# Optimization experiments

Measured on AMD Instinct MI355X. Metric: run time of the kernel, lower is better.

The kernel has to match this reference:

```python
import jax, jax.numpy as jnp
import numpy as np

N, D_IN, D_H = 8192, 512, 512


def setup_inputs() -> dict:
    key = jax.random.key(0)
    kH, kWq, kbq, kWk, kbk = jax.random.split(key, 5)
    s_in = 1.0 / np.sqrt(D_IN)
    return {
        "H": jax.random.normal(kH, (N, D_IN), dtype=jnp.float32),
        "Wq": jax.random.normal(kWq, (D_IN, D_H), dtype=jnp.float32) * s_in,
        "bq": jax.random.normal(kbq, (D_H,), dtype=jnp.float32) * 0.01,
        "Wk": jax.random.normal(kWk, (D_IN, D_H), dtype=jnp.float32) * s_in,
        "bk": jax.random.normal(kbk, (D_H,), dtype=jnp.float32) * 0.01,
    }


def reference(H, Wq, bq, Wk, bk):
    # H: [N, T]; Q, K: [N, d_h]
    Q = H @ Wq + bq
    K = H @ Wk + bk
    # A: [N, N] raw scores
    A = Q @ K.T
    n = A.shape[0]
    # torch.where(eye, 0, A): zero out the diagonal BEFORE scale/softmax
    A = A.at[jnp.arange(n), jnp.arange(n)].set(0.0)
    A = A / jnp.sqrt(jnp.asarray(K.shape[-1], A.dtype))
    A = jax.nn.softmax(A, axis=-1)
    # aggregate values (= H itself) and add residual
    return A @ H + H
```

## Files before the change

### kernel.cpp

```cpp
#include <hip/hip_runtime.h>
#include <cstdint>
#include <cstddef>

#define GLOBAL_AS __attribute__((address_space(1)))
#define LDS_AS __attribute__((address_space(3)))

typedef __attribute__((ext_vector_type(8))) short short8;
typedef __attribute__((ext_vector_type(4))) float floatx4;
typedef __attribute__((ext_vector_type(2))) long long2v;

#if defined(__has_builtin)
#if __has_builtin(__builtin_amdgcn_cvt_pk_fp8_f32)
#define HAVE_HW_FP8 1
#endif
#endif

static __device__ __forceinline__ unsigned short f2bf(float f) {
  uint32_t u = __builtin_bit_cast(uint32_t, f);
  u += 0x7fffu + ((u >> 16) & 1u);
  return (unsigned short)(u >> 16);
}

static __device__ __forceinline__ unsigned char f2fp8(float f) {
#ifdef HAVE_HW_FP8
  float c = fminf(fmaxf(f, -448.f), 448.f);
  return (unsigned char)(__builtin_amdgcn_cvt_pk_fp8_f32(c, 0.f, 0, false) & 0xff);
#else
  unsigned char s = 0;
  if (f < 0.f) { s = 0x80; f = -f; }
  if (f >= 448.f) return s | 0x7e;
  if (f < 0.015625f) { int r = (int)(f * 512.f + 0.5f); return s | (unsigned char)r; }
  uint32_t u = __builtin_bit_cast(uint32_t, f);
  int e = (int)((u >> 23) & 0xff) - 127;
  uint32_t keep = (u >> 20) & 7, rest = u & 0xfffffu;
  if (rest > 0x80000u || (rest == 0x80000u && (keep & 1))) ++keep;
  if (keep == 8) { keep = 0; ++e; }
  if (e > 8) return s | 0x7e;
  return s | (unsigned char)(((e + 7) << 3) | keep);
#endif
}

static __device__ __forceinline__ uint32_t pack4fp8(const float e[4]) {
#ifdef HAVE_HW_FP8
  const uint32_t p01 = (uint32_t)__builtin_amdgcn_cvt_pk_fp8_f32(e[0], e[1], 0, false);
  const uint32_t p23 = (uint32_t)__builtin_amdgcn_cvt_pk_fp8_f32(e[2], e[3], 0, false);
  return (p01 & 0xffffu) | (p23 << 16);
#else
  return (uint32_t)f2fp8(e[0]) | ((uint32_t)f2fp8(e[1]) << 8) |
         ((uint32_t)f2fp8(e[2]) << 16) | ((uint32_t)f2fp8(e[3]) << 24);
#endif
}

static __device__ __forceinline__ uint32_t gather_dword(uint32_t w, int quad, int l15) {
  const int src = quad * 16 + 4 * (l15 & 3);
  const int sh = (l15 >> 2) * 8;
  const uint32_t v0 = (uint32_t)__shfl((int)w, src);
  const uint32_t v1 = (uint32_t)__shfl((int)w, src + 1);
  const uint32_t v2 = (uint32_t)__shfl((int)w, src + 2);
  const uint32_t v3 = (uint32_t)__shfl((int)w, src + 3);
  return ((v0 >> sh) & 0xffu) | (((v1 >> sh) & 0xffu) << 8) |
         (((v2 >> sh) & 0xffu) << 16) | (((v3 >> sh) & 0xffu) << 24);
}

static __device__ __forceinline__ void wait_vm0() {
  __builtin_amdgcn_s_waitcnt(0x0f70);
}

__global__ __launch_bounds__(256) void transpose_h_kernel(
    const float* __restrict__ in, unsigned char* __restrict__ outT8,
    unsigned short* __restrict__ outN, int R, int C) {
  __shared__ float t[64][65];
  const int bc = blockIdx.x * 64;
  const int br = blockIdx.y * 64;
  const int tc = threadIdx.x & 63;
  const int tr = threadIdx.x >> 6;
  for (int r = tr; r < 64; r += 4) {
    const float v = in[(size_t)(br + r) * C + bc + tc];
    t[r][tc] = v;
    outN[(size_t)(br + r) * C + bc + tc] = f2bf(v);
  }
  __syncthreads();
  for (int r = tr; r < 64; r += 4)
    outT8[(size_t)(bc + r) * R + br + tc] = f2fp8(t[tc][r]);
}

__global__ __launch_bounds__(256) void transpose_w_kernel(
    const float* __restrict__ in, unsigned short* __restrict__ outT, int R, int C) {
  __shared__ float t[64][65];
  const int bc = blockIdx.x * 64;
  const int br = blockIdx.y * 64;
  const int tc = threadIdx.x & 63;
  const int tr = threadIdx.x >> 6;
  for (int r = tr; r < 64; r += 4)
    t[r][tc] = in[(size_t)(br + r) * C + bc + tc];
  __syncthreads();
  for (int r = tr; r < 64; r += 4)
    outT[(size_t)(bc + r) * R + br + tc] = f2bf(t[tc][r]);
}

__global__ __launch_bounds__(256) void pack_bias_kernel(
    const float* __restrict__ bq, const float* __restrict__ bk,
    float* __restrict__ bqk) {
  int i = blockIdx.x * 256 + threadIdx.x;
  bqk[i] = (i < 512) ? bq[i] : bk[i - 512];
}

__global__ __launch_bounds__(256, 4) void gemm_proj(
    const unsigned short* __restrict__ A,
    const unsigned short* __restrict__ Bt,
    int Ncols, int K,
    const float* __restrict__ bias,
    unsigned char* __restrict__ C8)
{
  __shared__ unsigned short As[2][128 * 32];
  __shared__ unsigned short Bs[2][128 * 32];

  const int tid  = threadIdx.x;
  const int lane = tid & 63;
  const int wave = tid >> 6;
  const int wr   = (wave >> 1) * 64;
  const int wc   = (wave & 1) * 64;
  const int quad = lane >> 4;
  const int l15  = lane & 15;
  const int bm   = blockIdx.y * 128;
  const int bn   = blockIdx.x * 128;

  const int c0 = tid, c1 = tid + 256;
  const int r0a = c0 >> 2, k0a = (c0 & 3) << 3;
  const int r1a = c1 >> 2, k1a = (c1 & 3) << 3;

  auto stage = [&](int kt, int b) {
    __builtin_amdgcn_global_load_lds(
        (const GLOBAL_AS void*)(A + (size_t)(bm + r0a) * K + kt + k0a),
        (LDS_AS void*)(&As[b][c0 * 8]), 16, 0, 0);
    __builtin_amdgcn_global_load_lds(
        (const GLOBAL_AS void*)(A + (size_t)(bm + r1a) * K + kt + k1a),
        (LDS_AS void*)(&As[b][c1 * 8]), 16, 0, 0);
    __builtin_amdgcn_global_load_lds(
        (const GLOBAL_AS void*)(Bt + (size_t)(bn + r0a) * K + kt + k0a),
        (LDS_AS void*)(&Bs[b][c0 * 8]), 16, 0, 0);
    __builtin_amdgcn_global_load_lds(
        (const GLOBAL_AS void*)(Bt + (size_t)(bn + r1a) * K + kt + k1a),
        (LDS_AS void*)(&Bs[b][c1 * 8]), 16, 0, 0);
  };

  floatx4 acc[4][4];
#pragma unroll
  for (int i = 0; i < 4; ++i)
#pragma unroll
    for (int j = 0; j < 4; ++j)
      acc[i][j] = (floatx4){0.f, 0.f, 0.f, 0.f};

  stage(0, 0);
  const int nIter = K >> 5;
  for (int it = 0; it < nIter; ++it) {
    const int b = it & 1;
    wait_vm0();
    __syncthreads();
    if (it + 1 < nIter) stage((it + 1) << 5, b ^ 1);

    short8 af[4], bfr[4];
#pragma unroll
    for (int i = 0; i < 4; ++i)
      af[i] = *(const short8*)(&As[b][(wr + i * 16 + l15) * 32 + quad * 8]);
#pragma unroll
    for (int j = 0; j < 4; ++j)
      bfr[j] = *(const short8*)(&Bs[b][(wc + j * 16 + l15) * 32 + quad * 8]);
#pragma unroll
    for (int i = 0; i < 4; ++i)
#pragma unroll
      for (int j = 0; j < 4; ++j)
        acc[i][j] = __builtin_amdgcn_mfma_f32_16x16x32_bf16(af[i], bfr[j], acc[i][j], 0, 0, 0);
  }

#pragma unroll
  for (int i = 0; i < 4; ++i) {
    const int rl = bm + wr + i * 16 + quad * 4;
#pragma unroll
    for (int r = 0; r < 4; ++r) {
      const int row = rl + r;
      float e[4];
#pragma unroll
      for (int j = 0; j < 4; ++j)
        e[j] = acc[i][j][r] + bias[bn + wc + j * 16 + l15];
      const uint32_t d = gather_dword(pack4fp8(e), quad, l15);
      *(uint32_t*)(C8 + (size_t)row * Ncols + bn + wc + 4 * l15) = d;
    }
  }
}

__global__ __launch_bounds__(512, 6) void gemm_qk8(
    const unsigned char* __restrict__ A,
    const unsigned char* __restrict__ Bt,
    int Ncols, int K, int lda, int ldb,
    float* __restrict__ lsum,
    int row0,
    unsigned char* __restrict__ P8)
{
  __shared__ unsigned char As[2][128 * 64];
  __shared__ unsigned char Bs[2][128 * 64];

  const int tid  = threadIdx.x;
  const int lane = tid & 63;
  const int wave = tid >> 6;
  const int wr   = (wave >> 1) * 32;
  const int wc   = (wave & 1) * 64;
  const int quad = lane >> 4;
  const int l15  = lane & 15;
  const int bm   = blockIdx.y * 128;
  const int bn   = blockIdx.x * 128;

  const int rS = tid >> 2, kS = (tid & 3) << 4;

  auto stage = [&](int kt, int b) {
    __builtin_amdgcn_global_load_lds(
        (const GLOBAL_AS void*)(A + (size_t)(bm + rS) * lda + kt + kS),
        (LDS_AS void*)(&As[b][tid * 16]), 16, 0, 0);
    __builtin_amdgcn_global_load_lds(
        (const GLOBAL_AS void*)(Bt + (size_t)(bn + rS) * ldb + kt + kS),
        (LDS_AS void*)(&Bs[b][tid * 16]), 16, 0, 0);
  };

  floatx4 acc[2][4];
#pragma unroll
  for (int i = 0; i < 2; ++i)
#pragma unroll
    for (int j = 0; j < 4; ++j)
      acc[i][j] = (floatx4){0.f, 0.f, 0.f, 0.f};

  stage(0, 0);
  const int nIter = K >> 6;
  for (int it = 0; it < nIter; ++it) {
    const int b = it & 1;
    wait_vm0();
    __syncthreads();
    if (it + 1 < nIter) stage((it + 1) << 6, b ^ 1);

    long2v af[2], bfr[4];
#pragma unroll
    for (int i = 0; i < 2; ++i)
      af[i] = *(const long2v*)(&As[b][(wr + i * 16 + l15) * 64 + quad * 16]);
#pragma unroll
    for (int j = 0; j < 4; ++j)
      bfr[j] = *(const long2v*)(&Bs[b][(wc + j * 16 + l15) * 64 + quad * 16]);
#pragma unroll
    for (int i = 0; i < 2; ++i)
#pragma unroll
      for (int j = 0; j < 4; ++j) {
        acc[i][j] = __builtin_amdgcn_mfma_f32_16x16x32_fp8_fp8(af[i].x, bfr[j].x, acc[i][j], 0, 0, 0);
        acc[i][j] = __builtin_amdgcn_mfma_f32_16x16x32_fp8_fp8(af[i].y, bfr[j].y, acc[i][j], 0, 0, 0);
      }
  }

  const float scale = 0.044194173824159216f;
#pragma unroll
  for (int i = 0; i < 2; ++i) {
    const int rl = bm + wr + i * 16 + quad * 4;
#pragma unroll
    for (int r = 0; r < 4; ++r) {
      const int row = rl + r;
      float e[4];
#pragma unroll
      for (int j = 0; j < 4; ++j) {
        const int col = bn + wc + j * 16 + l15;
        const float lg = ((row0 + row) == col) ? 0.f : acc[i][j][r] * scale;
        e[j] = fminf(__expf(lg), 448.f);
      }
      float rsum = (e[0] + e[1]) + (e[2] + e[3]);
      const uint32_t d = gather_dword(pack4fp8(e), quad, l15);
      *(uint32_t*)(P8 + (size_t)row * Ncols + bn + wc + 4 * l15) = d;
      rsum += __shfl_xor(rsum, 1);
      rsum += __shfl_xor(rsum, 2);
      rsum += __shfl_xor(rsum, 4);
      rsum += __shfl_xor(rsum, 8);
      if (l15 == 0) atomicAdd(&lsum[row0 + row], rsum);
    }
  }
}

template <bool DIRECT>
__global__ __launch_bounds__(256, 6) void gemm_pv8(
    const unsigned char* __restrict__ P,
    const unsigned char* __restrict__ Bt,
    int Kchunk,
    const float* __restrict__ lvec,
    const float* __restrict__ Hres,
    int row0,
    float* __restrict__ outp,
    size_t partStride)
{
  __shared__ unsigned char As[2][64 * 64];
  __shared__ unsigned char Bs[2][128 * 64];

  const int tid  = threadIdx.x;
  const int lane = tid & 63;
  const int wave = tid >> 6;
  const int wr   = (wave >> 1) * 32;
  const int wc   = (wave & 1) * 64;
  const int quad = lane >> 4;
  const int l15  = lane & 15;
  const int bm   = blockIdx.y * 64;
  const int bn   = blockIdx.x * 128;
  const int k0   = blockIdx.z * Kchunk;

  float* part = outp + (DIRECT ? 0 : (size_t)blockIdx.z * partStride);

  const int rA = tid >> 2,  kA = (tid & 3) << 4;
  const int cB1 = tid + 256;
  const int rB0 = tid >> 2, kB0 = (tid & 3) << 4;
  const int rB1 = cB1 >> 2, kB1 = (cB1 & 3) << 4;

  auto stage = [&](int kt, int b) {
    __builtin_amdgcn_global_load_lds(
        (const GLOBAL_AS void*)(P + (size_t)(bm + rA) * 8192 + kt + kA),
        (LDS_AS void*)(&As[b][tid * 16]), 16, 0, 0);
    __builtin_amdgcn_global_load_lds(
        (const GLOBAL_AS void*)(Bt + (size_t)(bn + rB0) * 8192 + kt + kB0),
        (LDS_AS void*)(&Bs[b][tid * 16]), 16, 0, 0);
    __builtin_amdgcn_global_load_lds(
        (const GLOBAL_AS void*)(Bt + (size_t)(bn + rB1) * 8192 + kt + kB1),
        (LDS_AS void*)(&Bs[b][cB1 * 16]), 16, 0, 0);
  };

  floatx4 acc[2][4];
#pragma unroll
  for (int i = 0; i < 2; ++i)
#pragma unroll
    for (int j = 0; j < 4; ++j)
      acc[i][j] = (floatx4){0.f, 0.f, 0.f, 0.f};

  stage(k0, 0);
  const int nIter = Kchunk >> 6;
  for (int it = 0; it < nIter; ++it) {
    const int b = it & 1;
    wait_vm0();
    __syncthreads();
    if (it + 1 < nIter) stage(k0 + ((it + 1) << 6), b ^ 1);

    long2v af[2], bfr[4];
#pragma unroll
    for (int i = 0; i < 2; ++i)
      af[i] = *(const long2v*)(&As[b][(wr + i * 16 + l15) * 64 + quad * 16]);
#pragma unroll
    for (int j = 0; j < 4; ++j)
      bfr[j] = *(const long2v*)(&Bs[b][(wc + j * 16 + l15) * 64 + quad * 16]);
#pragma unroll
    for (int i = 0; i < 2; ++i)
#pragma unroll
      for (int j = 0; j < 4; ++j) {
        acc[i][j] = __builtin_amdgcn_mfma_f32_16x16x32_fp8_fp8(af[i].x, bfr[j].x, acc[i][j], 0, 0, 0);
        acc[i][j] = __builtin_amdgcn_mfma_f32_16x16x32_fp8_fp8(af[i].y, bfr[j].y, acc[i][j], 0, 0, 0);
      }
  }

#pragma unroll
  for (int i = 0; i < 2; ++i) {
    const int rl = bm + wr + i * 16 + quad * 4;
#pragma unroll
    for (int j = 0; j < 4; ++j) {
      const int col = bn + wc + j * 16 + l15;
#pragma unroll
      for (int r = 0; r < 4; ++r) {
        const int row = rl + r;
        const float v = acc[i][j][r];
        if (DIRECT) {
          const int grow = row0 + row;
          part[(size_t)grow * 512 + col] =
              v / lvec[grow] + Hres[(size_t)grow * 512 + col];
        } else {
          part[(size_t)row * 512 + col] = v;
        }
      }
    }
  }
}

__global__ __launch_bounds__(256) void combine_kernel(
    const float* __restrict__ parts, size_t partStride, int S,
    const float* __restrict__ lvec, const float* __restrict__ Hres,
    float* __restrict__ out, int n4) {
  int i = blockIdx.x * 256 + threadIdx.x;
  if (i >= n4) return;
  float4 a = ((const float4*)parts)[i];
  for (int s = 1; s < S; ++s) {
    const float4 b = ((const float4*)(parts + (size_t)s * partStride))[i];
    a.x += b.x; a.y += b.y; a.z += b.z; a.w += b.w;
  }
  const int row = i >> 7;
  const float inv = 1.f / lvec[row];
  const float4 h = ((const float4*)Hres)[i];
  float4 o;
  o.x = a.x * inv + h.x;
  o.y = a.y * inv + h.y;
  o.z = a.z * inv + h.z;
  o.w = a.w * inv + h.w;
  ((float4*)out)[i] = o;
}

extern "C" void kernel_launch(void* const* d_in, const int* in_sizes, int n_in,
                              void* d_out, int out_size, void* d_ws, size_t ws_size,
                              hipStream_t stream) {
  const float* H  = (const float*)d_in[0];
  const float* Wq = (const float*)d_in[1];
  const float* bq = (const float*)d_in[2];
  const float* Wk = (const float*)d_in[3];
  const float* bk = (const float*)d_in[4];
  float* out = (float*)d_out;

  const int N = 8192, D = 512;

  char* ws = (char*)d_ws;
  size_t off = 0;
  auto alloc = [&](size_t bytes) { char* p = ws + off; off += bytes; return p; };
  unsigned short* Hb   = (unsigned short*)alloc((size_t)N * D * 2);
  unsigned char*  HbT8 = (unsigned char*)alloc((size_t)D * N);
  unsigned char*  QK8  = (unsigned char*)alloc((size_t)N * 2 * D);
  unsigned short* BqkT = (unsigned short*)alloc((size_t)2 * D * D * 2);
  float* bqk = (float*)alloc((size_t)2 * D * 4);
  float* l   = (float*)alloc((size_t)N * 4);
  const size_t base = off;
  unsigned char* P8 = (unsigned char*)(ws + base);

  const size_t pBytes = (size_t)N * N;
  const size_t partBytes = (size_t)N * D * 4;
  const size_t partStride = (size_t)N * D;
  const size_t avail = (ws_size > base) ? (ws_size - base) : 0;

  int S = 0;
  if (avail >= pBytes) {
    const size_t extra = avail - pBytes;
    S = (extra >= 2 * partBytes) ? 2 : 1;
  }
  float* parts = (float*)(ws + base + pBytes);

  hipMemsetAsync(l, 0, (size_t)N * 4, stream);
  transpose_h_kernel<<<dim3(D / 64, N / 64), 256, 0, stream>>>(H, HbT8, Hb, N, D);
  transpose_w_kernel<<<dim3(D / 64, D / 64), 256, 0, stream>>>(Wq, BqkT, D, D);
  transpose_w_kernel<<<dim3(D / 64, D / 64), 256, 0, stream>>>(Wk, BqkT + (size_t)D * D, D, D);
  pack_bias_kernel<<<dim3(4), 256, 0, stream>>>(bq, bk, bqk);

  gemm_proj<<<dim3(2 * D / 128, N / 128), 256, 0, stream>>>(
      Hb, BqkT, 2 * D, D, bqk, QK8);

  if (S >= 1) {
    gemm_qk8<<<dim3(N / 128, N / 128), 512, 0, stream>>>(
        QK8, QK8 + D, N, D, 2 * D, 2 * D, l, 0, P8);
    if (S == 1) {
      gemm_pv8<true><<<dim3(D / 128, N / 64, 1), 256, 0, stream>>>(
          P8, HbT8, N, l, H, 0, out, 0);
    } else {
      gemm_pv8<false><<<dim3(D / 128, N / 64, S), 256, 0, stream>>>(
          P8, HbT8, N / S, nullptr, nullptr, 0, parts, partStride);
      combine_kernel<<<dim3((N * D / 4 + 255) / 256), 256, 0, stream>>>(
          parts, partStride, S, l, H, out, N * D / 4);
    }
  } else {
    int maxRows = (int)(avail / (size_t)N);
    maxRows &= ~127;
    if (maxRows < 128) maxRows = 128;
    for (int r0 = 0; r0 < N; r0 += maxRows) {
      int rows = N - r0;
      if (rows > maxRows) rows = maxRows;
      gemm_qk8<<<dim3(N / 128, rows / 128), 512, 0, stream>>>(
          QK8 + (size_t)r0 * 2 * D, QK8 + D, N, D, 2 * D, 2 * D, l, r0, P8);
      gemm_pv8<true><<<dim3(D / 128, rows / 64, 1), 256, 0, stream>>>(
          P8, HbT8, N, l, H, r0, out, 0);
    }
  }
}
```

Measured before the change: 269.7 us.

## Switch QK and PV GEMMs to 16x16x128 scaled fp8 MFMA with swizzled LDS

Both fp8 GEMM kernels now use the MI355X scaled MFMA instruction (16x16x128 f8f6f4, unit scales) in place of pairs of 16x16x32 fp8 MFMAs. K-tiles grow to 128 with an XOR-swizzled LDS layout to avoid bank conflicts. LDS footprint doubles and occupancy hints drop. The goal is to cut MFMA instruction count and loop overhead and raise matrix throughput, at the cost of fewer resident blocks per CU.

After: 269.1 us. Within noise of the previous version (-0.2%).

```diff
diff --git a/kernel.cpp b/kernel.cpp
--- a/kernel.cpp
+++ b/kernel.cpp
@@ -7,7 +7,8 @@
 
 typedef __attribute__((ext_vector_type(8))) short short8;
 typedef __attribute__((ext_vector_type(4))) float floatx4;
-typedef __attribute__((ext_vector_type(2))) long long2v;
+typedef __attribute__((ext_vector_type(4))) int int4v;
+typedef __attribute__((ext_vector_type(8))) int int8v;
 
 #if defined(__has_builtin)
 #if __has_builtin(__builtin_amdgcn_cvt_pk_fp8_f32)
@@ -66,6 +67,22 @@
   __builtin_amdgcn_s_waitcnt(0x0f70);
 }
 
+static __device__ __forceinline__ int8v load_frag32(const unsigned char* base, int row, int quad) {
+  const int h = row & 7;
+  const int c0 = (2 * quad) ^ h;
+  const int c1 = (2 * quad + 1) ^ h;
+  const int4v lo = *(const int4v*)(base + row * 128 + c0 * 16);
+  const int4v hi = *(const int4v*)(base + row * 128 + c1 * 16);
+  int8v r;
+  r[0] = lo[0]; r[1] = lo[1]; r[2] = lo[2]; r[3] = lo[3];
+  r[4] = hi[0]; r[5] = hi[1]; r[6] = hi[2]; r[7] = hi[3];
+  return r;
+}
+
+static __device__ __forceinline__ floatx4 mx_mfma(int8v a, int8v b, floatx4 c) {
+  return __builtin_amdgcn_mfma_scale_f32_16x16x128_f8f6f4(a, b, c, 0, 0, 0, 0x7f, 0, 0x7f);
+}
+
 __global__ __launch_bounds__(256) void transpose_h_kernel(
     const float* __restrict__ in, unsigned char* __restrict__ outT8,
     unsigned short* __restrict__ outN, int R, int C) {
@@ -189,7 +206,7 @@
   }
 }
 
-__global__ __launch_bounds__(512, 6) void gemm_qk8(
+__global__ __launch_bounds__(512, 4) void gemm_qk8(
     const unsigned char* __restrict__ A,
     const unsigned char* __restrict__ Bt,
     int Ncols, int K, int lda, int ldb,
@@ -197,8 +214,8 @@
     int row0,
     unsigned char* __restrict__ P8)
 {
-  __shared__ unsigned char As[2][128 * 64];
-  __shared__ unsigned char Bs[2][128 * 64];
+  __shared__ unsigned char As[2][128 * 128];
+  __shared__ unsigned char Bs[2][128 * 128];
 
   const int tid  = threadIdx.x;
   const int lane = tid & 63;
@@ -210,15 +227,23 @@
   const int bm   = blockIdx.y * 128;
   const int bn   = blockIdx.x * 128;
 
-  const int rS = tid >> 2, kS = (tid & 3) << 4;
+  const int L0 = tid, L1 = tid + 512;
+  const int sr0 = L0 >> 3, sc0 = ((L0 & 7) ^ (sr0 & 7)) << 4;
+  const int sr1 = L1 >> 3, sc1 = ((L1 & 7) ^ (sr1 & 7)) << 4;
 
   auto stage = [&](int kt, int b) {
     __builtin_amdgcn_global_load_lds(
-        (const GLOBAL_AS void*)(A + (size_t)(bm + rS) * lda + kt + kS),
-        (LDS_AS void*)(&As[b][tid * 16]), 16, 0, 0);
-    __builtin_amdgcn_global_load_lds(
-        (const GLOBAL_AS void*)(Bt + (size_t)(bn + rS) * ldb + kt + kS),
-        (LDS_AS void*)(&Bs[b][tid * 16]), 16, 0, 0);
+        (const GLOBAL_AS void*)(A + (size_t)(bm + sr0) * lda + kt + sc0),
+        (LDS_AS void*)(&As[b][L0 * 16]), 16, 0, 0);
+    __builtin_amdgcn_global_load_lds(
+        (const GLOBAL_AS void*)(A + (size_t)(bm + sr1) * lda + kt + sc1),
+        (LDS_AS void*)(&As[b][L1 * 16]), 16, 0, 0);
+    __builtin_amdgcn_global_load_lds(
+        (const GLOBAL_AS void*)(Bt + (size_t)(bn + sr0) * ldb + kt + sc0),
+        (LDS_AS void*)(&Bs[b][L0 * 16]), 16, 0, 0);
+    __builtin_amdgcn_global_load_lds(
+        (const GLOBAL_AS void*)(Bt + (size_t)(bn + sr1) * ldb + kt + sc1),
+        (LDS_AS void*)(&Bs[b][L1 * 16]), 16, 0, 0);
   };
 
   floatx4 acc[2][4];
@@ -229,27 +254,21 @@
       acc[i][j] = (floatx4){0.f, 0.f, 0.f, 0.f};
 
   stage(0, 0);
-  const int nIter = K >> 6;
+  const int nIter = K >> 7;
   for (int it = 0; it < nIter; ++it) {
     const int b = it & 1;
     wait_vm0();
     __syncthreads();
-    if (it + 1 < nIter) stage((it + 1) << 6, b ^ 1);
-
-    long2v af[2], bfr[4];
-#pragma unroll
-    for (int i = 0; i < 2; ++i)
-      af[i] = *(const long2v*)(&As[b][(wr + i * 16 + l15) * 64 + quad * 16]);
-#pragma unroll
-    for (int j = 0; j < 4; ++j)
-      bfr[j] = *(const long2v*)(&Bs[b][(wc + j * 16 + l15) * 64 + quad * 16]);
-#pragma unroll
-    for (int i = 0; i < 2; ++i)
-#pragma unroll
-      for (int j = 0; j < 4; ++j) {
-        acc[i][j] = __builtin_amdgcn_mfma_f32_16x16x32_fp8_fp8(af[i].x, bfr[j].x, acc[i][j], 0, 0, 0);
-        acc[i][j] = __builtin_amdgcn_mfma_f32_16x16x32_fp8_fp8(af[i].y, bfr[j].y, acc[i][j], 0, 0, 0);
-      }
+    if (it + 1 < nIter) stage((it + 1) << 7, b ^ 1);
+
+    const int8v af0 = load_frag32(As[b], wr + l15, quad);
+    const int8v af1 = load_frag32(As[b], wr + 16 + l15, quad);
+#pragma unroll
+    for (int j = 0; j < 4; ++j) {
+      const int8v bf = load_frag32(Bs[b], wc + j * 16 + l15, quad);
+      acc[0][j] = mx_mfma(af0, bf, acc[0][j]);
+      acc[1][j] = mx_mfma(af1, bf, acc[1][j]);
+    }
   }
 
   const float scale = 0.044194173824159216f;
@@ -279,7 +298,7 @@
 }
 
 template <bool DIRECT>
-__global__ __launch_bounds__(256, 6) void gemm_pv8(
+__global__ __launch_bounds__(256, 3) void gemm_pv8(
     const unsigned char* __restrict__ P,
     const unsigned char* __restrict__ Bt,
     int Kchunk,
@@ -289,8 +308,8 @@
     float* __restrict__ outp,
     size_t partStride)
 {
-  __shared__ unsigned char As[2][64 * 64];
-  __shared__ unsigned char Bs[2][128 * 64];
+  __shared__ unsigned char As[2][64 * 128];
+  __shared__ unsigned char Bs[2][128 * 128];
 
   const int tid  = threadIdx.x;
   const int lane = tid & 63;
@@ -305,21 +324,34 @@
 
   float* part = outp + (DIRECT ? 0 : (size_t)blockIdx.z * partStride);
 
-  const int rA = tid >> 2,  kA = (tid & 3) << 4;
-  const int cB1 = tid + 256;
-  const int rB0 = tid >> 2, kB0 = (tid & 3) << 4;
-  const int rB1 = cB1 >> 2, kB1 = (cB1 & 3) << 4;
+  const int a0 = tid, a1 = tid + 256;
+  const int ar0 = a0 >> 3, ac0 = ((a0 & 7) ^ (ar0 & 7)) << 4;
+  const int ar1 = a1 >> 3, ac1 = ((a1 & 7) ^ (ar1 & 7)) << 4;
+  const int b0 = tid, b1 = tid + 256, b2 = tid + 512, b3 = tid + 768;
+  const int br0 = b0 >> 3, bc0 = ((b0 & 7) ^ (br0 & 7)) << 4;
+  const int br1 = b1 >> 3, bc1 = ((b1 & 7) ^ (br1 & 7)) << 4;
+  const int br2 = b2 >> 3, bc2 = ((b2 & 7) ^ (br2 & 7)) << 4;
+  const int br3 = b3 >> 3, bc3 = ((b3 & 7) ^ (br3 & 7)) << 4;
 
   auto stage = [&](int kt, int b) {
     __builtin_amdgcn_global_load_lds(
-        (const GLOBAL_AS void*)(P + (size_t)(bm + rA) * 8192 + kt + kA),
-        (LDS_AS void*)(&As[b][tid * 16]), 16, 0, 0);
-    __builtin_amdgcn_global_load_lds(
-        (const GLOBAL_AS void*)(Bt + (size_t)(bn + rB0) * 8192 + kt + kB0),
-        (LDS_AS void*)(&Bs[b][tid * 16]), 16, 0, 0);
-    __builtin_amdgcn_global_load_lds(
-        (const GLOBAL_AS void*)(Bt + (size_t)(bn + rB1) * 8192 + kt + kB1),
-        (LDS_AS void*)(&Bs[b][cB1 * 16]), 16, 0, 0);
+        (const GLOBAL_AS void*)(P + (size_t)(bm + ar0) * 8192 + kt + ac0),
+        (LDS_AS void*)(&As[b][a0 * 16]), 16, 0, 0);
+    __builtin_amdgcn_global_load_lds(
+        (const GLOBAL_AS void*)(P + (size_t)(bm + ar1) * 8192 + kt + ac1),
+        (LDS_AS void*)(&As[b][a1 * 16]), 16, 0, 0);
+    __builtin_amdgcn_global_load_lds(
+        (const GLOBAL_AS void*)(Bt + (size_t)(bn + br0) * 8192 + kt + bc0),
+        (LDS_AS void*)(&Bs[b][b0 * 16]), 16, 0, 0);
+    __builtin_amdgcn_global_load_lds(
+        (const GLOBAL_AS void*)(Bt + (size_t)(bn + br1) * 8192 + kt + bc1),
+        (LDS_AS void*)(&Bs[b][b1 * 16]), 16, 0, 0);
+    __builtin_amdgcn_global_load_lds(
+        (const GLOBAL_AS void*)(Bt + (size_t)(bn + br2) * 8192 + kt + bc2),
+        (LDS_AS void*)(&Bs[b][b2 * 16]), 16, 0, 0);
+    __builtin_amdgcn_global_load_lds(
+        (const GLOBAL_AS void*)(Bt + (size_t)(bn + br3) * 8192 + kt + bc3),
+        (LDS_AS void*)(&Bs[b][b3 * 16]), 16, 0, 0);
   };
 
   floatx4 acc[2][4];
@@ -330,27 +362,21 @@
       acc[i][j] = (floatx4){0.f, 0.f, 0.f, 0.f};
 
   stage(k0, 0);
-  const int nIter = Kchunk >> 6;
+  const int nIter = Kchunk >> 7;
   for (int it = 0; it < nIter; ++it) {
     const int b = it & 1;
     wait_vm0();
     __syncthreads();
-    if (it + 1 < nIter) stage(k0 + ((it + 1) << 6), b ^ 1);
-
-    long2v af[2], bfr[4];
-#pragma unroll
-    for (int i = 0; i < 2; ++i)
-      af[i] = *(const long2v*)(&As[b][(wr + i * 16 + l15) * 64 + quad * 16]);
-#pragma unroll
-    for (int j = 0; j < 4; ++j)
-      bfr[j] = *(const long2v*)(&Bs[b][(wc + j * 16 + l15) * 64 + quad * 16]);
-#pragma unroll
-    for (int i = 0; i < 2; ++i)
-#pragma unroll
-      for (int j = 0; j < 4; ++j) {
-        acc[i][j] = __builtin_amdgcn_mfma_f32_16x16x32_fp8_fp8(af[i].x, bfr[j].x, acc[i][j], 0, 0, 0);
-        acc[i][j] = __builtin_amdgcn_mfma_f32_16x16x32_fp8_fp8(af[i].y, bfr[j].y, acc[i][j], 0, 0, 0);
-      }
+    if (it + 1 < nIter) stage(k0 + ((it + 1) << 7), b ^ 1);
+
+    const int8v af0 = load_frag32(As[b], wr + l15, quad);
+    const int8v af1 = load_frag32(As[b], wr + 16 + l15, quad);
+#pragma unroll
+    for (int j = 0; j < 4; ++j) {
+      const int8v bf = load_frag32(Bs[b], wc + j * 16 + l15, quad);
+      acc[0][j] = mx_mfma(af0, bf, acc[0][j]);
+      acc[1][j] = mx_mfma(af1, bf, acc[1][j]);
+    }
   }
 
 #pragma unroll
```
